# Kernel optimization log

Measured on AMD Instinct MI355X. Metric: run time of the kernel, lower is better.

## Reference

```python
import jax, jax.numpy as jnp
import numpy as np

N_HEAD = 8
TOTAL_DIM = 64   # trans dim: num_node*f_dim + arV_dim = 15*4 + 4
F_DIM = 4        # node_feature_dim
NUM_NODE = 15
EPS = 1e-5


def _ln(x, g, b):
    m = jnp.mean(x, axis=-1, keepdims=True)
    v = jnp.var(x, axis=-1, keepdims=True)
    return (x - m) * jax.lax.rsqrt(v + EPS) * g + b


def setup_inputs() -> dict:
    key = jax.random.key(0)
    B, T, C, L, V = 4, 1024, 1024, 4, 100
    ks = jax.random.split(key, 16)
    g = lambda k, sh, s=0.02: jax.random.normal(k, sh, jnp.float32) * s
    return {
        'x': jax.random.normal(ks[0], (B, T, C), jnp.float32),
        'attn_bias': jax.random.normal(ks[1], (N_HEAD, NUM_NODE, NUM_NODE), jnp.float32),
        'pos_emb': g(ks[2], (1, T, C)),
        'Wq': g(ks[3], (L, C, C)), 'bq': jnp.zeros((L, C), jnp.float32),
        'Wk': g(ks[4], (L, C, C)), 'bk': jnp.zeros((L, C), jnp.float32),
        'Wv': g(ks[5], (L, C, C)), 'bv': jnp.zeros((L, C), jnp.float32),
        'Wp': g(ks[6], (L, C, C)), 'bp': jnp.zeros((L, C), jnp.float32),
        'ln1_g': jnp.ones((L, C), jnp.float32), 'ln1_b': jnp.zeros((L, C), jnp.float32),
        'ln2_g': jnp.ones((L, C), jnp.float32), 'ln2_b': jnp.zeros((L, C), jnp.float32),
        'w1': g(ks[7], (L, C, 4 * C)), 'b1': jnp.zeros((L, 4 * C), jnp.float32),
        'w2': g(ks[8], (L, 4 * C, C)), 'b2': jnp.zeros((L, C), jnp.float32),
        'lnf_g': jnp.ones((C,), jnp.float32), 'lnf_b': jnp.zeros((C,), jnp.float32),
        'head_w': g(ks[9], (TOTAL_DIM, V + 1, C)),
    }


def reference(x, attn_bias, pos_emb, Wq, bq, Wk, bk, Wv, bv, Wp, bp,
              ln1_g, ln1_b, ln2_g, ln2_b, w1, b1, w2, b2, lnf_g, lnf_b, head_w):
    B, T, C = x.shape
    L = Wq.shape[0]
    hd = C // N_HEAD
    scale = 1.0 / np.sqrt(hd).astype(np.float32)

    # expand graph bias: bias[h, i*f+a, j*f+b] = attn_bias[h, i, j]
    d = NUM_NODE * F_DIM
    bias = jnp.repeat(jnp.repeat(attn_bias, F_DIM, axis=1), F_DIM, axis=2)  # [nh, d, d]
    pbias = jnp.zeros((N_HEAD, T, T), x.dtype).at[:, :d, :d].set(bias)      # [nh, T, T]

    # causal mask with every TOTAL_DIM-th column disabled
    mask = jnp.tril(jnp.ones((T, T), bool))
    mask = mask & ((jnp.arange(T) % TOTAL_DIM) != TOTAL_DIM - 1)[None, :]

    h = x + pos_emb[:, :T]
    neg_inf = jnp.asarray(-jnp.inf, x.dtype)
    for l in range(L):  # fixed small layer count
        a = _ln(h, ln1_g[l], ln1_b[l])
        q = (a @ Wq[l] + bq[l]).reshape(B, T, N_HEAD, hd).transpose(0, 2, 1, 3)
        k = (a @ Wk[l] + bk[l]).reshape(B, T, N_HEAD, hd).transpose(0, 2, 1, 3)
        v = (a @ Wv[l] + bv[l]).reshape(B, T, N_HEAD, hd).transpose(0, 2, 1, 3)
        att = jnp.einsum('bhid,bhjd->bhij', q, k) * scale + pbias[None]
        att = jnp.where(mask[None, None], att, neg_inf)
        att = jax.nn.softmax(att, axis=-1)
        y = jnp.einsum('bhij,bhjd->bhid', att, v).transpose(0, 2, 1, 3).reshape(B, T, C)
        h = h + y @ Wp[l] + bp[l]
        a2 = _ln(h, ln2_g[l], ln2_b[l])
        h = h + jax.nn.gelu(a2 @ w1[l] + b1[l], approximate=False) @ w2[l] + b2[l]

    h = _ln(h, lnf_g, lnf_b)
    # pad_to_full_observation + EinLinear head
    n_pad = (-T) % TOTAL_DIM
    hp = jnp.pad(h, ((0, 0), (0, n_pad), (0, 0))).reshape(-1, TOTAL_DIM, C)
    logits = jnp.einsum('eoi,bei->beo', head_w, hp)
    return logits.reshape(B, T + n_pad, -1)[:, :T]
```

## Files before the change

kernel.cpp:

```cpp
#include <hip/hip_runtime.h>
#include <cstdint>

#define DEV __device__ __forceinline__

typedef unsigned short u16;
typedef __attribute__((ext_vector_type(8))) short bf16x8;
typedef __attribute__((ext_vector_type(4))) unsigned short u16x4;
typedef __attribute__((ext_vector_type(4))) float f32x4;

typedef __attribute__((address_space(1))) const void GV;
typedef __attribute__((address_space(3))) void LV;

DEV float b2f(u16 u) { uint32_t i = ((uint32_t)u) << 16; return __builtin_bit_cast(float, i); }
DEV u16 f2b(float f) {
    uint32_t i = __builtin_bit_cast(uint32_t, f);
    return (u16)((i + 0x7fffu + ((i >> 16) & 1u)) >> 16);
}
DEV void load_lds16(const void* g, void* l) {
    __builtin_amdgcn_global_load_lds((GV*)g, (LV*)l, 16, 0, 0);
}

__global__ __launch_bounds__(256) void k_addpos(const float* __restrict__ x,
                                                const float* __restrict__ pos,
                                                float* __restrict__ h) {
    size_t i = (size_t)blockIdx.x * 256 + threadIdx.x;
    f32x4 a = *(const f32x4*)(x + i * 4);
    f32x4 p = *(const f32x4*)(pos + ((i * 4) & 1048575));
    a += p;
    *(f32x4*)(h + i * 4) = a;
}

__global__ __launch_bounds__(256) void k_transcvt(const float* __restrict__ W,
                                                  u16* __restrict__ WT, int K, int N,
                                                  size_t ozs) {
    __shared__ float t[32][33];
    size_t zin = (size_t)blockIdx.z * K * N, zout = (size_t)blockIdx.z * ozs;
    int n0 = blockIdx.x * 32, k0 = blockIdx.y * 32;
    int r = threadIdx.x >> 3, c = (threadIdx.x & 7) << 2;
    f32x4 v = *(const f32x4*)(W + zin + (size_t)(k0 + r) * N + n0 + c);
    t[r][c] = v[0]; t[r][c + 1] = v[1]; t[r][c + 2] = v[2]; t[r][c + 3] = v[3];
    __syncthreads();
    u16x4 o;
    o[0] = f2b(t[c][r]); o[1] = f2b(t[c + 1][r]); o[2] = f2b(t[c + 2][r]); o[3] = f2b(t[c + 3][r]);
    *(u16x4*)(WT + zout + (size_t)(n0 + r) * K + k0 + c) = o;
}

__global__ __launch_bounds__(256) void k_cvt(const float* __restrict__ in,
                                             u16* __restrict__ out, int n4) {
    int i = blockIdx.x * 256 + threadIdx.x;
    if (i < n4) {
        f32x4 v = *(const f32x4*)(in + (size_t)i * 4);
        u16x4 o; o[0] = f2b(v[0]); o[1] = f2b(v[1]); o[2] = f2b(v[2]); o[3] = f2b(v[3]);
        *(u16x4*)(out + (size_t)i * 4) = o;
    }
}

__global__ __launch_bounds__(256) void k_packb(const float* __restrict__ bq,
                                               const float* __restrict__ bk,
                                               const float* __restrict__ bv,
                                               float* __restrict__ bqkv) {
    int l = blockIdx.x;
    for (int i = threadIdx.x; i < 1024; i += 256) {
        bqkv[l * 3072 + i]        = bq[l * 1024 + i];
        bqkv[l * 3072 + 1024 + i] = bk[l * 1024 + i];
        bqkv[l * 3072 + 2048 + i] = bv[l * 1024 + i];
    }
}

__global__ __launch_bounds__(256) void k_ln(const float* __restrict__ in,
                                            const float* __restrict__ g,
                                            const float* __restrict__ bta,
                                            u16* __restrict__ out) {
    int row = blockIdx.x, tid = threadIdx.x;
    const float* rp = in + (size_t)row * 1024;
    f32x4 v = *(const f32x4*)(rp + tid * 4);
    float s = v[0] + v[1] + v[2] + v[3];
    float ss = v[0] * v[0] + v[1] * v[1] + v[2] * v[2] + v[3] * v[3];
    #pragma unroll
    for (int off = 32; off; off >>= 1) { s += __shfl_down(s, off); ss += __shfl_down(ss, off); }
    __shared__ float rs[4], rss[4];
    int wave = tid >> 6, lane = tid & 63;
    if (!lane) { rs[wave] = s; rss[wave] = ss; }
    __syncthreads();
    float ts = rs[0] + rs[1] + rs[2] + rs[3];
    float tss = rss[0] + rss[1] + rss[2] + rss[3];
    float mean = ts * (1.0f / 1024.0f);
    float var = tss * (1.0f / 1024.0f) - mean * mean;
    float rstd = rsqrtf(var + 1e-5f);
    f32x4 gv = *(const f32x4*)(g + tid * 4);
    f32x4 bv = *(const f32x4*)(bta + tid * 4);
    u16x4 o;
    #pragma unroll
    for (int j = 0; j < 4; ++j) o[j] = f2b((v[j] - mean) * rstd * gv[j] + bv[j]);
    *(u16x4*)(out + (size_t)row * 1024 + tid * 4) = o;
}

__global__ __launch_bounds__(256) void k_gemmr(const u16* __restrict__ A,
                                               const u16* __restrict__ BT,
                                               const float* __restrict__ bias,
                                               float* __restrict__ H,
                                               int M, int N, int K) {
    __shared__ __align__(16) u16 As[2][64 * 64];
    __shared__ __align__(16) u16 Bs[2][64 * 64];
    const int tid = threadIdx.x, lane = tid & 63, wave = tid >> 6;
    const int wy = wave >> 1, wx = wave & 1;
    const int lcol = lane & 15, lrow = lane >> 4;

    const int nbx = gridDim.x, nwg = nbx * gridDim.y;
    int id = blockIdx.y * nbx + blockIdx.x;
    int q = nwg >> 3, r = nwg & 7;
    int xcd = id & 7, pos = id >> 3;
    int nid = (xcd < r ? xcd * (q + 1) : r * (q + 1) + (xcd - r) * q) + pos;
    const int m0 = (nid / nbx) * 64, n0 = (nid % nbx) * 64;
    const int NT = K >> 6;

    f32x4 acc[2][2] = {};

    auto stage = [&](int buf, int kt) {
        int k0 = kt << 6;
        #pragma unroll
        for (int it = 0; it < 2; ++it) {
            int c = it * 256 + tid;
            int row = c >> 3, s = (c & 7) ^ (row & 7);
            load_lds16(A + (size_t)(m0 + row) * K + k0 + s * 8,
                       &As[buf][(it * 256 + wave * 64) * 8]);
        }
        #pragma unroll
        for (int it = 0; it < 2; ++it) {
            int c = it * 256 + tid;
            int row = c >> 3, s = (c & 7) ^ (row & 7);
            load_lds16(BT + (size_t)(n0 + row) * K + k0 + s * 8,
                       &Bs[buf][(it * 256 + wave * 64) * 8]);
        }
    };

    stage(0, 0);
    for (int kt = 0; kt < NT; ++kt) {
        __syncthreads();
        if (kt + 1 < NT) stage((kt + 1) & 1, kt + 1);
        const u16* ab = As[kt & 1];
        const u16* bb = Bs[kt & 1];
        #pragma unroll
        for (int kc = 0; kc < 2; ++kc) {
            bf16x8 af[2], bfr[2];
            #pragma unroll
            for (int mi = 0; mi < 2; ++mi) {
                int mrow = wy * 32 + mi * 16 + lcol;
                int s = (kc * 4 + lrow) ^ (mrow & 7);
                af[mi] = *(const bf16x8*)(ab + mrow * 64 + s * 8);
            }
            #pragma unroll
            for (int ni = 0; ni < 2; ++ni) {
                int nrow = wx * 32 + ni * 16 + lcol;
                int s = (kc * 4 + lrow) ^ (nrow & 7);
                bfr[ni] = *(const bf16x8*)(bb + nrow * 64 + s * 8);
            }
            #pragma unroll
            for (int mi = 0; mi < 2; ++mi)
                #pragma unroll
                for (int ni = 0; ni < 2; ++ni)
                    acc[mi][ni] = __builtin_amdgcn_mfma_f32_16x16x32_bf16(af[mi], bfr[ni], acc[mi][ni], 0, 0, 0);
        }
    }

    #pragma unroll
    for (int mi = 0; mi < 2; ++mi) {
        #pragma unroll
        for (int ni = 0; ni < 2; ++ni) {
            int col = n0 + wx * 32 + ni * 16 + lcol;
            float bcol = bias[col];
            #pragma unroll
            for (int r2 = 0; r2 < 4; ++r2) {
                int row = m0 + wy * 32 + mi * 16 + lrow * 4 + r2;
                float* o = H + (size_t)row * N + col;
                *o = *o + acc[mi][ni][r2] + bcol;
            }
        }
    }
}

template <int EPI>
__global__ __launch_bounds__(512) void k_g128(const u16* __restrict__ A,
                                              const u16* __restrict__ BT,
                                              const float* __restrict__ bias,
                                              u16* __restrict__ Cout,
                                              int M, int N, int K) {
    __shared__ __align__(16) u16 As[2][4096];
    __shared__ __align__(16) u16 Bs[2][8192];
    const int tid = threadIdx.x, lane = tid & 63, wave = tid >> 6;
    const int wy = wave >> 2, wx = wave & 3;
    const int lcol = lane & 15, lrow = lane >> 4;

    const int nbx = gridDim.x, nwg = nbx * gridDim.y;
    int id = blockIdx.y * nbx + blockIdx.x;
    int q = nwg >> 3, r = nwg & 7;
    int xcd = id & 7, pos = id >> 3;
    int nid = (xcd < r ? xcd * (q + 1) : r * (q + 1) + (xcd - r) * q) + pos;
    const int m0 = (nid / nbx) * 128, n0 = (nid % nbx) * 256;
    const int NT = K >> 5;

    f32x4 acc[4][4] = {};

    auto stage = [&](int buf, int kt) {
        int k0 = kt << 5;
        {
            int c = tid;
            int row = c >> 2, s = (c & 3) ^ ((row >> 1) & 3);
            load_lds16(A + (size_t)(m0 + row) * K + k0 + s * 8,
                       &As[buf][(wave * 64) * 8]);
        }
        #pragma unroll
        for (int it = 0; it < 2; ++it) {
            int c = it * 512 + tid;
            int row = c >> 2, s = (c & 3) ^ ((row >> 1) & 3);
            load_lds16(BT + (size_t)(n0 + row) * K + k0 + s * 8,
                       &Bs[buf][(it * 512 + wave * 64) * 8]);
        }
    };

    stage(0, 0);
    for (int kt = 0; kt < NT; ++kt) {
        __syncthreads();
        if (kt + 1 < NT) stage((kt + 1) & 1, kt + 1);
        const u16* ab = As[kt & 1];
        const u16* bb = Bs[kt & 1];
        bf16x8 bfr[4];
        #pragma unroll
        for (int ni = 0; ni < 4; ++ni) {
            int nrow = wx * 64 + ni * 16 + lcol;
            bfr[ni] = *(const bf16x8*)(bb + nrow * 32 + ((lrow ^ ((nrow >> 1) & 3)) * 8));
        }
        #pragma unroll
        for (int mi = 0; mi < 4; ++mi) {
            int mrow = wy * 64 + mi * 16 + lcol;
            bf16x8 af = *(const bf16x8*)(ab + mrow * 32 + ((lrow ^ ((mrow >> 1) & 3)) * 8));
            #pragma unroll
            for (int ni = 0; ni < 4; ++ni)
                acc[mi][ni] = __builtin_amdgcn_mfma_f32_16x16x32_bf16(af, bfr[ni], acc[mi][ni], 0, 0, 0);
        }
    }

    #pragma unroll
    for (int mi = 0; mi < 4; ++mi) {
        #pragma unroll
        for (int ni = 0; ni < 4; ++ni) {
            int col = n0 + wx * 64 + ni * 16 + lcol;
            float bcol = bias[col];
            #pragma unroll
            for (int r2 = 0; r2 < 4; ++r2) {
                int row = m0 + wy * 64 + mi * 16 + lrow * 4 + r2;
                float val = acc[mi][ni][r2] + bcol;
                if constexpr (EPI == 1)
                    val = 0.5f * val * (1.0f + erff(val * 0.70710678118654752f));
                Cout[(size_t)row * N + col] = f2b(val);
            }
        }
    }
}

__global__ __launch_bounds__(256) void k_attn(const u16* __restrict__ qkv,
                                              const float* __restrict__ abias,
                                              u16* __restrict__ yb) {
    __shared__ __align__(16) u16 Ks[2][64 * 128];
    __shared__ __align__(16) u16 Vt[2][128 * 64];
    __shared__ __align__(16) u16 Ps[4][16 * 72];

    const int idx = blockIdx.x;
    const int half = idx >> 8, u = idx & 255;
    const int qt = half ? (15 - (u & 15)) : (u & 15);
    const int h = (u >> 4) & 7;
    const int b = (u >> 7) + half * 2;

    const int tid = threadIdx.x, wave = tid >> 6, lane = tid & 63;
    const int lcol = lane & 15, lrow = lane >> 4;
    const int q0 = qt * 64 + wave * 16;
    const size_t base = (size_t)b * 1024 * 3072 + h * 128;
    const u16* qp = qkv + base;
    const u16* kp = qkv + base + 1024;
    const u16* vp = qkv + base + 2048;
    u16* psw = Ps[wave];
    const int j4 = tid & 15, d8 = tid >> 4;

    bf16x8 aq[4];
    #pragma unroll
    for (int df = 0; df < 4; ++df)
        aq[df] = *(const bf16x8*)(qp + (size_t)(q0 + lcol) * 3072 + df * 32 + lrow * 8);

    f32x4 o[8];
    #pragma unroll
    for (int i = 0; i < 8; ++i) o[i] = f32x4{0.f, 0.f, 0.f, 0.f};
    float mrun[4], lrun[4];
    #pragma unroll
    for (int r = 0; r < 4; ++r) { mrun[r] = -__builtin_inff(); lrun[r] = 0.f; }

    const float scale = 0.08838834764831845f;
    const int nt = qt + 1;

    auto k_issue = [&](int buf, int t) {
        const int j0 = t * 64;
        #pragma unroll
        for (int it = 0; it < 4; ++it) {
            int c = it * 256 + wave * 64 + lane;
            int row = c >> 4, slot = c & 15;
            int sslot = slot ^ (row & 7);
            load_lds16(kp + (size_t)(j0 + row) * 3072 + sslot * 8,
                       &Ks[buf][(it * 256 + wave * 64) * 8]);
        }
    };
    auto v_issue = [&](int t, bf16x8* vr) {
        const int j0 = t * 64;
        #pragma unroll
        for (int r = 0; r < 4; ++r)
            vr[r] = *(const bf16x8*)(vp + (size_t)(j0 + j4 * 4 + r) * 3072 + d8 * 8);
    };
    auto v_write = [&](int buf, const bf16x8* vr) {
        #pragma unroll
        for (int i = 0; i < 8; ++i) {
            int d = d8 * 8 + i;
            u16x4 w;
            w[0] = (u16)vr[0][i]; w[1] = (u16)vr[1][i]; w[2] = (u16)vr[2][i]; w[3] = (u16)vr[3][i];
            *(u16x4*)(&Vt[buf][d * 64 + ((j4 * 4) ^ (i << 3))]) = w;
        }
    };

    bf16x8 v0r[4];
    k_issue(0, 0);
    v_issue(0, v0r);
    v_write(0, v0r);

    for (int t = 0; t < nt; ++t) {
        __syncthreads();
        const int cur = t & 1, nxt = cur ^ 1;
        const bool more = (t + 1 < nt);
        bf16x8 vn[4];
        if (more) { k_issue(nxt, t + 1); v_issue(t + 1, vn); }

        const u16* ks = Ks[cur];
        const u16* vt = Vt[cur];
        const int j0 = t * 64;

        f32x4 S[4];
        #pragma unroll
        for (int sub = 0; sub < 4; ++sub) {
            const int row = sub * 16 + lcol;
            const int sw = row & 7;
            f32x4 s = {};
            #pragma unroll
            for (int df = 0; df < 4; ++df) {
                bf16x8 kf = *(const bf16x8*)(ks + row * 128 + ((df * 4 + lrow) ^ sw) * 8);
                s = __builtin_amdgcn_mfma_f32_16x16x32_bf16(aq[df], kf, s, 0, 0, 0);
            }
            S[sub] = s;
        }

        float p[4][4], tmax[4];
        #pragma unroll
        for (int r = 0; r < 4; ++r) tmax[r] = -__builtin_inff();
        #pragma unroll
        for (int sub = 0; sub < 4; ++sub) {
            const int kj = j0 + sub * 16 + lcol;
            #pragma unroll
            for (int r = 0; r < 4; ++r) {
                const int qi = q0 + lrow * 4 + r;
                float v = S[sub][r] * scale;
                if (qi < 60 && kj < 60) v += abias[(h * 15 + (qi >> 2)) * 15 + (kj >> 2)];
                v = ((kj <= qi) && ((kj & 63) != 63)) ? v : -__builtin_inff();
                p[sub][r] = v;
                tmax[r] = fmaxf(tmax[r], v);
            }
        }
        #pragma unroll
        for (int off = 1; off < 16; off <<= 1)
            #pragma unroll
            for (int r = 0; r < 4; ++r) tmax[r] = fmaxf(tmax[r], __shfl_xor(tmax[r], off));
        float alpha[4], rsum[4];
        #pragma unroll
        for (int r = 0; r < 4; ++r) {
            float mnew = fmaxf(mrun[r], tmax[r]);
            alpha[r] = __expf(mrun[r] - mnew);
            mrun[r] = mnew;
            float acc = 0.f;
            #pragma unroll
            for (int sub = 0; sub < 4; ++sub) { p[sub][r] = __expf(p[sub][r] - mnew); acc += p[sub][r]; }
            rsum[r] = acc;
        }
        #pragma unroll
        for (int off = 1; off < 16; off <<= 1)
            #pragma unroll
            for (int r = 0; r < 4; ++r) rsum[r] += __shfl_xor(rsum[r], off);
        #pragma unroll
        for (int r = 0; r < 4; ++r) lrun[r] = lrun[r] * alpha[r] + rsum[r];
        #pragma unroll
        for (int i = 0; i < 8; ++i)
            #pragma unroll
            for (int r = 0; r < 4; ++r) o[i][r] *= alpha[r];

        #pragma unroll
        for (int sub = 0; sub < 4; ++sub)
            #pragma unroll
            for (int r = 0; r < 4; ++r)
                psw[(lrow * 4 + r) * 72 + sub * 16 + lcol] = f2b(p[sub][r]);

        #pragma unroll
        for (int kt = 0; kt < 2; ++kt) {
            bf16x8 pa = *(const bf16x8*)(psw + lcol * 72 + kt * 32 + lrow * 8);
            #pragma unroll
            for (int of = 0; of < 8; ++of) {
                const int d = of * 16 + lcol;
                bf16x8 vf = *(const bf16x8*)(vt + d * 64 + ((kt * 32 + lrow * 8) ^ ((d & 7) << 3)));
                o[of] = __builtin_amdgcn_mfma_f32_16x16x32_bf16(pa, vf, o[of], 0, 0, 0);
            }
        }

        if (more) v_write(nxt, vn);
    }

    u16* yp = yb + (size_t)b * 1024 * 1024 + h * 128;
    #pragma unroll
    for (int of = 0; of < 8; ++of)
        #pragma unroll
        for (int r = 0; r < 4; ++r) {
            int row = q0 + lrow * 4 + r;
            yp[(size_t)row * 1024 + of * 16 + lcol] = f2b(o[of][r] / lrun[r]);
        }
}

__global__ __launch_bounds__(256) void k_head(const u16* __restrict__ hln,
                                              const u16* __restrict__ hw16,
                                              float* __restrict__ out) {
    const int e = blockIdx.x, bq = blockIdx.y;
    const int lane = threadIdx.x & 63, wave = threadIdx.x >> 6;
    const int lcol = lane & 15, lrow = lane >> 4;

    const u16* ap = hln + ((size_t)bq * 1024 + lcol * 64 + e) * 1024 + lrow * 8;
    const int nt0 = wave, nt1 = wave + 4;
    const int oo0 = nt0 * 16 + lcol, oo1 = nt1 * 16 + lcol;
    const bool v0 = oo0 < 101;
    const bool has1 = nt1 < 7;
    const bool v1 = has1 && (oo1 < 101);
    const u16* bp0 = hw16 + ((size_t)e * 101 + (v0 ? oo0 : 0)) * 1024 + lrow * 8;
    const u16* bp1 = hw16 + ((size_t)e * 101 + (v1 ? oo1 : 0)) * 1024 + lrow * 8;

    f32x4 acc0 = {}, acc1 = {};
    #pragma unroll 4
    for (int kt = 0; kt < 32; ++kt) {
        bf16x8 af = *(const bf16x8*)(ap + kt * 32);
        bf16x8 b0 = {};
        if (v0) b0 = *(const bf16x8*)(bp0 + kt * 32);
        acc0 = __builtin_amdgcn_mfma_f32_16x16x32_bf16(af, b0, acc0, 0, 0, 0);
        if (has1) {
            bf16x8 b1 = {};
            if (v1) b1 = *(const bf16x8*)(bp1 + kt * 32);
            acc1 = __builtin_amdgcn_mfma_f32_16x16x32_bf16(af, b1, acc1, 0, 0, 0);
        }
    }

    #pragma unroll
    for (int r = 0; r < 4; ++r) {
        size_t row = (size_t)bq * 1024 + (lrow * 4 + r) * 64 + e;
        if (v0) out[row * 101 + oo0] = acc0[r];
        if (v1) out[row * 101 + oo1] = acc1[r];
    }
}

extern "C" void kernel_launch(void* const* d_in, const int* in_sizes, int n_in,
                              void* d_out, int out_size, void* d_ws, size_t ws_size,
                              hipStream_t stream) {
    (void)in_sizes; (void)n_in; (void)out_size; (void)ws_size;
    const float* x     = (const float*)d_in[0];
    const float* abias = (const float*)d_in[1];
    const float* pos   = (const float*)d_in[2];
    const float* Wq    = (const float*)d_in[3];
    const float* bq    = (const float*)d_in[4];
    const float* Wk    = (const float*)d_in[5];
    const float* bk    = (const float*)d_in[6];
    const float* Wv    = (const float*)d_in[7];
    const float* bv    = (const float*)d_in[8];
    const float* Wp    = (const float*)d_in[9];
    const float* bp    = (const float*)d_in[10];
    const float* ln1g  = (const float*)d_in[11];
    const float* ln1b  = (const float*)d_in[12];
    const float* ln2g  = (const float*)d_in[13];
    const float* ln2b  = (const float*)d_in[14];
    const float* w1    = (const float*)d_in[15];
    const float* b1    = (const float*)d_in[16];
    const float* w2    = (const float*)d_in[17];
    const float* b2    = (const float*)d_in[18];
    const float* lnfg  = (const float*)d_in[19];
    const float* lnfb  = (const float*)d_in[20];
    const float* hw    = (const float*)d_in[21];
    float* out = (float*)d_out;

    char* ws = (char*)d_ws;
    size_t off = 0;
    auto alloc = [&](size_t bytes) { void* p = ws + off; off += (bytes + 255) & ~(size_t)255; return p; };
    float* H    = (float*)alloc(4096ull * 1024 * 4);
    u16* ABF    = (u16*)alloc(4096ull * 1024 * 2);
    char* R     = (char*)alloc(4096ull * 4096 * 2);
    u16* QKV    = (u16*)R;
    u16* YB     = (u16*)(R + 4096ull * 3072 * 2);
    u16* MB     = (u16*)R;
    u16* WQKV   = (u16*)alloc(4ull * 3072 * 1024 * 2);
    u16* WPT    = (u16*)alloc(4ull * 1024 * 1024 * 2);
    u16* W1T    = (u16*)alloc(4ull * 1024 * 4096 * 2);
    u16* W2T    = (u16*)alloc(4ull * 4096 * 1024 * 2);
    u16* HW16   = (u16*)alloc(64ull * 101 * 1024 * 2);
    float* BQKV = (float*)alloc(4ull * 3072 * 4);

    dim3 blk(256);
    const size_t QS = 3072ull * 1024;
    k_transcvt<<<dim3(32, 32, 4), blk, 0, stream>>>(Wq, WQKV,                    1024, 1024, QS);
    k_transcvt<<<dim3(32, 32, 4), blk, 0, stream>>>(Wk, WQKV + 1024ull * 1024,   1024, 1024, QS);
    k_transcvt<<<dim3(32, 32, 4), blk, 0, stream>>>(Wv, WQKV + 2048ull * 1024,   1024, 1024, QS);
    k_transcvt<<<dim3(32, 32, 4), blk, 0, stream>>>(Wp, WPT, 1024, 1024, 1048576);
    k_transcvt<<<dim3(128, 32, 4), blk, 0, stream>>>(w1, W1T, 1024, 4096, 4194304);
    k_transcvt<<<dim3(32, 128, 4), blk, 0, stream>>>(w2, W2T, 4096, 1024, 4194304);
    k_cvt<<<dim3(64 * 101 * 1024 / 4 / 256), blk, 0, stream>>>(hw, HW16, 64 * 101 * 1024 / 4);
    k_packb<<<dim3(4), blk, 0, stream>>>(bq, bk, bv, BQKV);
    k_addpos<<<dim3(4096), blk, 0, stream>>>(x, pos, H);

    for (int l = 0; l < 4; ++l) {
        k_ln<<<dim3(4096), blk, 0, stream>>>(H, ln1g + l * 1024, ln1b + l * 1024, ABF);
        k_g128<0><<<dim3(12, 32), dim3(512), 0, stream>>>(ABF, WQKV + (size_t)l * QS, BQKV + l * 3072, QKV, 4096, 3072, 1024);
        k_attn<<<dim3(512), blk, 0, stream>>>(QKV, abias, YB);
        k_gemmr<<<dim3(16, 64), blk, 0, stream>>>(YB, WPT + (size_t)l * 1048576, bp + l * 1024, H, 4096, 1024, 1024);
        k_ln<<<dim3(4096), blk, 0, stream>>>(H, ln2g + l * 1024, ln2b + l * 1024, ABF);
        k_g128<1><<<dim3(16, 32), dim3(512), 0, stream>>>(ABF, W1T + (size_t)l * 4194304, b1 + l * 4096, MB, 4096, 4096, 1024);
        k_gemmr<<<dim3(16, 64), blk, 0, stream>>>(MB, W2T + (size_t)l * 4194304, b2 + l * 1024, H, 4096, 1024, 4096);
    }
    k_ln<<<dim3(4096), blk, 0, stream>>>(H, lnfg, lnfb, ABF);
    k_head<<<dim3(64, 4), blk, 0, stream>>>(ABF, HW16, out);
}
```

Measured before the change: 996.2 us.

## Replace 128x256 GEMM with 256x256 triple-buffered ping-pong pipelined kernel

The QKV and FC1 GEMMs now use a 256x256 output tile per 512-thread block instead of 128x256, so each wave holds 8x4 accumulators and more work is reused per LDS load. A three-stage LDS buffer prefetches two k-steps ahead. Each k-step is split into two halves, with explicit barriers, waitcnts and s_setprio so global-to-LDS copies overlap the MFMA bursts. The grid halves to 192 and 256 blocks, which risks lower occupancy and tail imbalance on 256 CUs, and register pressure rises.

```diff
diff --git a/kernel.cpp b/kernel.cpp
--- a/kernel.cpp
+++ b/kernel.cpp
@@ -180,13 +180,13 @@
 }
 
 template <int EPI>
-__global__ __launch_bounds__(512) void k_g128(const u16* __restrict__ A,
-                                              const u16* __restrict__ BT,
-                                              const float* __restrict__ bias,
-                                              u16* __restrict__ Cout,
-                                              int M, int N, int K) {
-    __shared__ __align__(16) u16 As[2][4096];
-    __shared__ __align__(16) u16 Bs[2][8192];
+__global__ __launch_bounds__(512, 2) void k_g8p(const u16* __restrict__ A,
+                                                const u16* __restrict__ BT,
+                                                const float* __restrict__ bias,
+                                                u16* __restrict__ Cout,
+                                                int M, int N, int K) {
+    __shared__ __align__(16) u16 As[3][256 * 32];
+    __shared__ __align__(16) u16 Bs[3][256 * 32];
     const int tid = threadIdx.x, lane = tid & 63, wave = tid >> 6;
     const int wy = wave >> 2, wx = wave & 3;
     const int lcol = lane & 15, lrow = lane >> 4;
@@ -196,59 +196,102 @@
     int q = nwg >> 3, r = nwg & 7;
     int xcd = id & 7, pos = id >> 3;
     int nid = (xcd < r ? xcd * (q + 1) : r * (q + 1) + (xcd - r) * q) + pos;
-    const int m0 = (nid / nbx) * 128, n0 = (nid % nbx) * 256;
+    const int m0 = (nid / nbx) * 256, n0 = (nid % nbx) * 256;
     const int NT = K >> 5;
 
-    f32x4 acc[4][4] = {};
-
-    auto stage = [&](int buf, int kt) {
+    f32x4 acc[8][4] = {};
+
+    auto stageA = [&](int bi, int kt) {
         int k0 = kt << 5;
-        {
-            int c = tid;
+        #pragma unroll
+        for (int it = 0; it < 2; ++it) {
+            int c = it * 512 + tid;
             int row = c >> 2, s = (c & 3) ^ ((row >> 1) & 3);
             load_lds16(A + (size_t)(m0 + row) * K + k0 + s * 8,
-                       &As[buf][(wave * 64) * 8]);
-        }
+                       &As[bi][(it * 512 + wave * 64) * 8]);
+        }
+    };
+    auto stageB = [&](int bi, int kt) {
+        int k0 = kt << 5;
         #pragma unroll
         for (int it = 0; it < 2; ++it) {
             int c = it * 512 + tid;
             int row = c >> 2, s = (c & 3) ^ ((row >> 1) & 3);
             load_lds16(BT + (size_t)(n0 + row) * K + k0 + s * 8,
-                       &Bs[buf][(it * 512 + wave * 64) * 8]);
+                       &Bs[bi][(it * 512 + wave * 64) * 8]);
         }
     };
 
-    stage(0, 0);
-    for (int kt = 0; kt < NT; ++kt) {
-        __syncthreads();
-        if (kt + 1 < NT) stage((kt + 1) & 1, kt + 1);
-        const u16* ab = As[kt & 1];
-        const u16* bb = Bs[kt & 1];
-        bf16x8 bfr[4];
+    stageA(0, 0); stageB(0, 0);
+    stageA(1, 1); stageB(1, 1);
+    asm volatile("s_waitcnt vmcnt(4)" ::: "memory");
+    __builtin_amdgcn_sched_barrier(0);
+    __builtin_amdgcn_s_barrier();
+
+    int buf = 0;
+    for (int t = 0; t < NT; ++t) {
+        const u16* ab = As[buf];
+        const u16* bb = Bs[buf];
+        int pb = buf + 2; if (pb >= 3) pb -= 3;
+        const bool pre = (t + 2 < NT);
+
+        bf16x8 bfr[4], af[4];
         #pragma unroll
         for (int ni = 0; ni < 4; ++ni) {
-            int nrow = wx * 64 + ni * 16 + lcol;
-            bfr[ni] = *(const bf16x8*)(bb + nrow * 32 + ((lrow ^ ((nrow >> 1) & 3)) * 8));
+            int rw = wx * 64 + ni * 16 + lcol;
+            bfr[ni] = *(const bf16x8*)(bb + rw * 32 + ((lrow ^ ((rw >> 1) & 3)) * 8));
         }
         #pragma unroll
         for (int mi = 0; mi < 4; ++mi) {
-            int mrow = wy * 64 + mi * 16 + lcol;
-            bf16x8 af = *(const bf16x8*)(ab + mrow * 32 + ((lrow ^ ((mrow >> 1) & 3)) * 8));
+            int rw = wy * 128 + mi * 16 + lcol;
+            af[mi] = *(const bf16x8*)(ab + rw * 32 + ((lrow ^ ((rw >> 1) & 3)) * 8));
+        }
+        if (pre) stageA(pb, t + 2);
+        __builtin_amdgcn_s_barrier();
+        asm volatile("s_waitcnt lgkmcnt(0)" ::: "memory");
+        __builtin_amdgcn_sched_barrier(0);
+        __builtin_amdgcn_s_setprio(1);
+        #pragma unroll
+        for (int mi = 0; mi < 4; ++mi)
             #pragma unroll
             for (int ni = 0; ni < 4; ++ni)
-                acc[mi][ni] = __builtin_amdgcn_mfma_f32_16x16x32_bf16(af, bfr[ni], acc[mi][ni], 0, 0, 0);
-        }
-    }
-
-    #pragma unroll
-    for (int mi = 0; mi < 4; ++mi) {
+                acc[mi][ni] = __builtin_amdgcn_mfma_f32_16x16x32_bf16(af[mi], bfr[ni], acc[mi][ni], 0, 0, 0);
+        __builtin_amdgcn_s_setprio(0);
+        __builtin_amdgcn_s_barrier();
+
+        #pragma unroll
+        for (int mi = 0; mi < 4; ++mi) {
+            int rw = wy * 128 + (mi + 4) * 16 + lcol;
+            af[mi] = *(const bf16x8*)(ab + rw * 32 + ((lrow ^ ((rw >> 1) & 3)) * 8));
+        }
+        if (pre) stageB(pb, t + 2);
+        __builtin_amdgcn_s_barrier();
+        asm volatile("s_waitcnt lgkmcnt(0)" ::: "memory");
+        __builtin_amdgcn_sched_barrier(0);
+        __builtin_amdgcn_s_setprio(1);
+        #pragma unroll
+        for (int mi = 0; mi < 4; ++mi)
+            #pragma unroll
+            for (int ni = 0; ni < 4; ++ni)
+                acc[mi + 4][ni] = __builtin_amdgcn_mfma_f32_16x16x32_bf16(af[mi], bfr[ni], acc[mi + 4][ni], 0, 0, 0);
+        __builtin_amdgcn_s_setprio(0);
+        if (pre) { asm volatile("s_waitcnt vmcnt(4)" ::: "memory"); }
+        else     { asm volatile("s_waitcnt vmcnt(0)" ::: "memory"); }
+        __builtin_amdgcn_sched_barrier(0);
+        __builtin_amdgcn_s_barrier();
+
+        buf = buf + 1; if (buf >= 3) buf -= 3;
+    }
+
+    #pragma unroll
+    for (int mi = 0; mi < 8; ++mi) {
         #pragma unroll
         for (int ni = 0; ni < 4; ++ni) {
             int col = n0 + wx * 64 + ni * 16 + lcol;
             float bcol = bias[col];
             #pragma unroll
             for (int r2 = 0; r2 < 4; ++r2) {
-                int row = m0 + wy * 64 + mi * 16 + lrow * 4 + r2;
+                int row = m0 + wy * 128 + mi * 16 + lrow * 4 + r2;
                 float val = acc[mi][ni][r2] + bcol;
                 if constexpr (EPI == 1)
                     val = 0.5f * val * (1.0f + erff(val * 0.70710678118654752f));
@@ -521,11 +564,11 @@
 
     for (int l = 0; l < 4; ++l) {
         k_ln<<<dim3(4096), blk, 0, stream>>>(H, ln1g + l * 1024, ln1b + l * 1024, ABF);
-        k_g128<0><<<dim3(12, 32), dim3(512), 0, stream>>>(ABF, WQKV + (size_t)l * QS, BQKV + l * 3072, QKV, 4096, 3072, 1024);
+        k_g8p<0><<<dim3(12, 16), dim3(512), 0, stream>>>(ABF, WQKV + (size_t)l * QS, BQKV + l * 3072, QKV, 4096, 3072, 1024);
         k_attn<<<dim3(512), blk, 0, stream>>>(QKV, abias, YB);
         k_gemmr<<<dim3(16, 64), blk, 0, stream>>>(YB, WPT + (size_t)l * 1048576, bp + l * 1024, H, 4096, 1024, 1024);
         k_ln<<<dim3(4096), blk, 0, stream>>>(H, ln2g + l * 1024, ln2b + l * 1024, ABF);
-        k_g128<1><<<dim3(16, 32), dim3(512), 0, stream>>>(ABF, W1T + (size_t)l * 4194304, b1 + l * 4096, MB, 4096, 4096, 1024);
+        k_g8p<1><<<dim3(16, 16), dim3(512), 0, stream>>>(ABF, W1T + (size_t)l * 4194304, b1 + l * 4096, MB, 4096, 4096, 1024);
         k_gemmr<<<dim3(16, 64), blk, 0, stream>>>(MB, W2T + (size_t)l * 4194304, b2 + l * 1024, H, 4096, 1024, 4096);
     }
     k_ln<<<dim3(4096), blk, 0, stream>>>(H, lnfg, lnfb, ABF);
```

After: 1.025 ms. 2.9% more time.
